# Optimization experiments

Hardware: AMD Instinct MI355X
Metric: run time of the kernel (lower is better)

## Reference

```python
import jax, jax.numpy as jnp
import numpy as np

B, S, D_IN, D_OUT, H = 4, 2048, 1024, 1024, 16
HD = D_OUT // H  # head_dim = 64


def setup_inputs() -> dict:
    key = jax.random.key(0)
    ks = jax.random.split(key, 9)
    sc_in = 1.0 / np.sqrt(D_IN)
    sc_out = 1.0 / np.sqrt(D_OUT)
    return {
        "x": jax.random.normal(ks[0], (B, S, D_IN), dtype=jnp.float32),
        "Wq": jax.random.normal(ks[1], (D_IN, D_OUT), dtype=jnp.float32) * sc_in,
        "bq": jax.random.normal(ks[2], (D_OUT,), dtype=jnp.float32) * 0.01,
        "Wk": jax.random.normal(ks[3], (D_IN, D_OUT), dtype=jnp.float32) * sc_in,
        "bk": jax.random.normal(ks[4], (D_OUT,), dtype=jnp.float32) * 0.01,
        "Wv": jax.random.normal(ks[5], (D_IN, D_OUT), dtype=jnp.float32) * sc_in,
        "bv": jax.random.normal(ks[6], (D_OUT,), dtype=jnp.float32) * 0.01,
        "Wo": jax.random.normal(ks[7], (D_OUT, D_OUT), dtype=jnp.float32) * sc_out,
        "bo": jax.random.normal(ks[8], (D_OUT,), dtype=jnp.float32) * 0.01,
    }


def reference(x, Wq, bq, Wk, bk, Wv, bv, Wo, bo):
    b, s, _ = x.shape
    # QKV projections -> [b, h, s, hd]
    def proj(W, bias):
        return (x @ W + bias).reshape(b, s, H, HD).transpose(0, 2, 1, 3)
    q, k, v = proj(Wq, bq), proj(Wk, bk), proj(Wv, bv)
    # scaled scores [b, h, s, s] with causal mask (future positions -> -inf)
    scores = jnp.einsum("bhqd,bhkd->bhqk", q, k) / jnp.sqrt(jnp.float32(HD))
    causal = jnp.triu(jnp.ones((s, s), dtype=bool), k=1)
    scores = jnp.where(causal, -jnp.inf, scores)
    attn = jax.nn.softmax(scores, axis=-1)  # dropout p=0.0 -> identity
    ctx = jnp.einsum("bhqk,bhkd->bhqd", attn, v)
    ctx = ctx.transpose(0, 2, 1, 3).reshape(b, s, D_OUT)
    return ctx @ Wo + bo
```

## Files before the change

### kernel.cpp

```cpp
#include <hip/hip_runtime.h>
#include <hip/hip_bf16.h>

#define B_   4
#define S_   2048
#define H_   16
#define HD_  64
#define D_   1024
#define M_   (B_ * S_)
#define N3_  3072

typedef unsigned short u16;
typedef __bf16 bf16x8 __attribute__((ext_vector_type(8)));
typedef float  f32x4  __attribute__((ext_vector_type(4)));
typedef unsigned short u16x8 __attribute__((ext_vector_type(8)));
typedef unsigned short u16x4 __attribute__((ext_vector_type(4)));

__device__ __forceinline__ float b2f(u16 u) {
    unsigned int x = ((unsigned int)u) << 16;
    return __builtin_bit_cast(float, x);
}
__device__ __forceinline__ u16 f2b(float f) {
    unsigned int x = __builtin_bit_cast(unsigned int, f);
    x += 0x7fffu + ((x >> 16) & 1u);
    return (u16)(x >> 16);
}
__device__ __forceinline__ u16 f2bt(float f) {
    return (u16)(__builtin_bit_cast(unsigned int, f) >> 16);
}

typedef const __attribute__((address_space(1))) unsigned int* gas_u32p;
typedef __attribute__((address_space(3))) unsigned int* las_u32p;
__device__ __forceinline__ void gl_lds16(const u16* g, u16* lds_base) {
    __builtin_amdgcn_global_load_lds((gas_u32p)g, (las_u32p)lds_base, 16, 0, 0);
}

__global__ __launch_bounds__(256) void cvt_k(const float* __restrict__ in,
                                             u16* __restrict__ out) {
    size_t i = ((size_t)blockIdx.x * 256 + threadIdx.x) * 8;
    float4 a = *(const float4*)(in + i);
    float4 b = *(const float4*)(in + i + 4);
    *(u16x8*)(out + i) = u16x8{f2b(a.x), f2b(a.y), f2b(a.z), f2b(a.w),
                               f2b(b.x), f2b(b.y), f2b(b.z), f2b(b.w)};
}

__global__ __launch_bounds__(256) void transpose4_k(
    const float* __restrict__ w0, const float* __restrict__ w1,
    const float* __restrict__ w2, const float* __restrict__ w3,
    u16* __restrict__ oqkv, u16* __restrict__ owo, float scale0) {
    __shared__ u16 t[32][33];
    const int z = blockIdx.z;
    const float* in = (z == 0) ? w0 : (z == 1) ? w1 : (z == 2) ? w2 : w3;
    u16* out = (z < 3) ? oqkv + (size_t)z * D_ * D_ : owo;
    const float sc = (z == 0) ? scale0 : 1.0f;
    const int x0 = blockIdx.x * 32, y0 = blockIdx.y * 32;
    const int tx = threadIdx.x & 31, ty = threadIdx.x >> 5;
#pragma unroll
    for (int i = 0; i < 32; i += 8)
        t[ty + i][tx] = f2b(in[(size_t)(y0 + ty + i) * D_ + x0 + tx] * sc);
    __syncthreads();
#pragma unroll
    for (int i = 0; i < 32; i += 8)
        out[(size_t)(x0 + ty + i) * D_ + y0 + tx] = t[tx][ty + i];
}

#define BM 128
#define BN 128
#define BK 64

template <int MODE>
__global__ __launch_bounds__(256) void gemm_core(
    const u16* __restrict__ A, const u16* __restrict__ Bt,
    const float* __restrict__ b0, const float* __restrict__ b1,
    const float* __restrict__ b2, float cscale,
    void* __restrict__ O0, void* __restrict__ O1, void* __restrict__ O2,
    int M, int N, int K)
{
    __shared__ __align__(16) u16 As[BM * BK];
    __shared__ __align__(16) u16 Bs[BN * BK];

    const int tid  = threadIdx.x;
    const int lane = tid & 63;
    const int wave = tid >> 6;
    const int wr = wave >> 1, wc = wave & 1;
    const int l15 = lane & 15, quad = lane >> 4;
    const int m0 = blockIdx.x * BM, n0 = blockIdx.y * BN;
    const int r8 = lane >> 3;
    const int csw = ((lane & 7) ^ r8) * 8;

    f32x4 acc[4][4] = {};

    for (int k0 = 0; k0 < K; k0 += BK) {
#pragma unroll
        for (int i = 0; i < 4; ++i) {
            const int row = wave * 32 + i * 8 + r8;
            gl_lds16(A  + (size_t)(m0 + row) * K + k0 + csw,
                     As + (wave * 32 + i * 8) * BK);
            gl_lds16(Bt + (size_t)(n0 + row) * K + k0 + csw,
                     Bs + (wave * 32 + i * 8) * BK);
        }
        __syncthreads();
        bf16x8 af[4][2], bfr[4][2];
#pragma unroll
        for (int t = 0; t < 4; ++t) {
            const u16* ap = As + (wr * 64 + t * 16 + l15) * BK;
            const u16* bp = Bs + (wc * 64 + t * 16 + l15) * BK;
            const int s7 = l15 & 7;
            af[t][0]  = *(const bf16x8*)(ap + ((quad    ) ^ s7) * 8);
            af[t][1]  = *(const bf16x8*)(ap + ((quad + 4) ^ s7) * 8);
            bfr[t][0] = *(const bf16x8*)(bp + ((quad    ) ^ s7) * 8);
            bfr[t][1] = *(const bf16x8*)(bp + ((quad + 4) ^ s7) * 8);
        }
#pragma unroll
        for (int mt = 0; mt < 4; ++mt)
#pragma unroll
            for (int nt = 0; nt < 4; ++nt) {
                acc[mt][nt] = __builtin_amdgcn_mfma_f32_16x16x32_bf16(
                    af[mt][0], bfr[nt][0], acc[mt][nt], 0, 0, 0);
                acc[mt][nt] = __builtin_amdgcn_mfma_f32_16x16x32_bf16(
                    af[mt][1], bfr[nt][1], acc[mt][nt], 0, 0, 0);
            }
        __syncthreads();
    }

#pragma unroll
    for (int nt = 0; nt < 4; ++nt) {
        const int col = n0 + wc * 64 + nt * 16 + l15;
        if constexpr (MODE == 1) {
            const float bv = b0[col];
#pragma unroll
            for (int mt = 0; mt < 4; ++mt) {
                const int rbase = m0 + wr * 64 + mt * 16 + quad * 4;
#pragma unroll
                for (int r2 = 0; r2 < 4; ++r2)
                    ((float*)O0)[(size_t)(rbase + r2) * N + col] =
                        acc[mt][nt][r2] + bv;
            }
        } else {
            const int qidx = col >> 10, ncol = col & (D_ - 1);
            const float bv = (qidx == 0) ? b0[ncol] * cscale
                           : (qidx == 1) ? b1[ncol] : b2[ncol];
#pragma unroll
            for (int mt = 0; mt < 4; ++mt) {
                const int rbase = m0 + wr * 64 + mt * 16 + quad * 4;
                if (qidx == 2) {
                    const int bidx = rbase >> 11, s = rbase & (S_ - 1);
                    const int hh = ncol >> 6, hd = ncol & 63;
                    u16x4 pk{f2b(acc[mt][nt][0] + bv), f2b(acc[mt][nt][1] + bv),
                             f2b(acc[mt][nt][2] + bv), f2b(acc[mt][nt][3] + bv)};
                    *(u16x4*)((u16*)O2 +
                        (((size_t)(bidx * H_ + hh)) * HD_ + hd) * S_ + s) = pk;
                } else {
                    u16* dst = (qidx == 0) ? (u16*)O0 : (u16*)O1;
#pragma unroll
                    for (int r2 = 0; r2 < 4; ++r2)
                        dst[(size_t)(rbase + r2) * D_ + ncol] =
                            f2b(acc[mt][nt][r2] + bv);
                }
            }
        }
    }
}

__global__ __launch_bounds__(256) void attn_mfma_k(
    const u16* __restrict__ Qm, const u16* __restrict__ Km,
    const u16* __restrict__ Vtg, u16* __restrict__ Om)
{
    __shared__ __align__(16) u16 Kbuf[2][64 * 64];
    __shared__ __align__(16) u16 Vbuf[2][64 * 64];
    __shared__ __align__(16) u16 Ps[4][16 * 64];

    const int tid  = threadIdx.x;
    const int lane = tid & 63;
    const int wave = tid >> 6;
    const int l15  = lane & 15;
    const int quad = lane >> 4;
    const int bh = blockIdx.x, b = bh >> 4, h = bh & (H_ - 1);
    const int j  = blockIdx.y;
    const int dg[4] = { j, 15 - j, 16 + j, 31 - j };

    const u16* Qg = Qm + (size_t)b * S_ * D_ + h * HD_;
    const u16* Kg = Km + (size_t)b * S_ * D_ + h * HD_;
    const u16* Vg = Vtg + ((size_t)(b * H_ + h)) * HD_ * S_;

    bf16x8 qf[4][2];
#pragma unroll
    for (int qs = 0; qs < 4; ++qs) {
        const u16* qp = Qg + (size_t)(dg[qs] * 64 + wave * 16 + l15) * D_ + quad * 8;
        qf[qs][0] = *(const bf16x8*)qp;
        qf[qs][1] = *(const bf16x8*)(qp + 32);
    }

    f32x4 of[4][4] = {};
    float lacc[4] = {0.f, 0.f, 0.f, 0.f};
    u16* pw = Ps[wave];
    const int qloc = wave * 16 + l15;
    const int r8 = lane >> 3;
    const int csw = ((lane & 7) ^ r8) * 8;

    auto stage = [&](int t, int bsel) {
        u16* kb = Kbuf[bsel];
        u16* vb = Vbuf[bsel];
#pragma unroll
        for (int i = 0; i < 2; ++i) {
            const int row = wave * 16 + i * 8 + r8;
            gl_lds16(Kg + (size_t)(t * 64 + row) * D_ + csw,
                     kb + (wave * 16 + i * 8) * 64);
            gl_lds16(Vg + (size_t)row * S_ + t * 64 + csw,
                     vb + (wave * 16 + i * 8) * 64);
        }
    };

    bf16x8 kf[4][2], vf[4][2];

    auto pass = [&](const bf16x8 (&q)[2], f32x4 (&o)[4], float& la, bool domask) {
        f32x4 sf[4];
#pragma unroll
        for (int kt = 0; kt < 4; ++kt) {
            f32x4 a = {};
            a = __builtin_amdgcn_mfma_f32_16x16x32_bf16(kf[kt][0], q[0], a, 0, 0, 0);
            a = __builtin_amdgcn_mfma_f32_16x16x32_bf16(kf[kt][1], q[1], a, 0, 0, 0);
            sf[kt] = a;
        }
        float ls = 0.f;
        u16 pb[16];
        if (domask) {
#pragma unroll
            for (int kt = 0; kt < 4; ++kt)
#pragma unroll
                for (int r = 0; r < 4; ++r) {
                    float v = sf[kt][r];
                    if (kt * 16 + quad * 4 + r > qloc) v = -INFINITY;
                    float p = __builtin_amdgcn_exp2f(v);
                    ls += p; pb[kt * 4 + r] = f2bt(p);
                }
        } else {
#pragma unroll
            for (int kt = 0; kt < 4; ++kt)
#pragma unroll
                for (int r = 0; r < 4; ++r) {
                    float p = __builtin_amdgcn_exp2f(sf[kt][r]);
                    ls += p; pb[kt * 4 + r] = f2bt(p);
                }
        }
        la += ls;
#pragma unroll
        for (int kt = 0; kt < 4; ++kt) {
            const int g = kt * 16 + quad * 4;
            const int pos = ((g >> 3) ^ (l15 & 7)) * 8 + (g & 7);
            *(u16x4*)(pw + l15 * 64 + pos) =
                u16x4{pb[kt * 4], pb[kt * 4 + 1], pb[kt * 4 + 2], pb[kt * 4 + 3]};
        }
        bf16x8 pf0 = *(const bf16x8*)(pw + l15 * 64 + ((quad    ) ^ (l15 & 7)) * 8);
        bf16x8 pf1 = *(const bf16x8*)(pw + l15 * 64 + ((quad + 4) ^ (l15 & 7)) * 8);
#pragma unroll
        for (int dt = 0; dt < 4; ++dt) {
            o[dt] = __builtin_amdgcn_mfma_f32_16x16x32_bf16(vf[dt][0], pf0, o[dt], 0, 0, 0);
            o[dt] = __builtin_amdgcn_mfma_f32_16x16x32_bf16(vf[dt][1], pf1, o[dt], 0, 0, 0);
        }
    };

    const int T = 32 - j;
    stage(0, 0);
    for (int t = 0; t < T; ++t) {
        __syncthreads();
        if (t + 1 < T) stage(t + 1, (t + 1) & 1);
        const u16* kb = Kbuf[t & 1];
        const u16* vb = Vbuf[t & 1];
#pragma unroll
        for (int kt = 0; kt < 4; ++kt) {
            const u16* kp = kb + (kt * 16 + l15) * 64;
            const u16* vp = vb + (kt * 16 + l15) * 64;
            const int s7 = l15 & 7;
            kf[kt][0] = *(const bf16x8*)(kp + ((quad    ) ^ s7) * 8);
            kf[kt][1] = *(const bf16x8*)(kp + ((quad + 4) ^ s7) * 8);
            vf[kt][0] = *(const bf16x8*)(vp + ((quad    ) ^ s7) * 8);
            vf[kt][1] = *(const bf16x8*)(vp + ((quad + 4) ^ s7) * 8);
        }
        if (t <= dg[0]) pass(qf[0], of[0], lacc[0], t == dg[0]);
        if (t <= dg[1]) pass(qf[1], of[1], lacc[1], t == dg[1]);
        if (t <= dg[2]) pass(qf[2], of[2], lacc[2], t == dg[2]);
        if (t <= dg[3]) pass(qf[3], of[3], lacc[3], t == dg[3]);
    }

    auto epi = [&](const f32x4 (&o)[4], float la, int dgq) {
        float ls = la;
        ls += __shfl_xor(ls, 16);
        ls += __shfl_xor(ls, 32);
        const float inv = 1.f / ls;
#pragma unroll
        for (int dt = 0; dt < 4; ++dt) {
            const int g = dt * 16 + quad * 4;
            const int pos = ((g >> 3) ^ (l15 & 7)) * 8 + (g & 7);
            *(u16x4*)(pw + l15 * 64 + pos) =
                u16x4{f2b(o[dt][0] * inv), f2b(o[dt][1] * inv),
                      f2b(o[dt][2] * inv), f2b(o[dt][3] * inv)};
        }
        const int r  = lane >> 2;
        const int cp = lane & 3;
        u16x8 o0 = *(const u16x8*)(pw + r * 64 + ((2 * cp    ) ^ (r & 7)) * 8);
        u16x8 o1 = *(const u16x8*)(pw + r * 64 + ((2 * cp + 1) ^ (r & 7)) * 8);
        u16* op = Om + ((size_t)(b * S_ + dgq * 64 + wave * 16 + r)) * D_ + h * 64 + cp * 16;
        *(u16x8*)op = o0;
        *(u16x8*)(op + 8) = o1;
    };
    epi(of[0], lacc[0], dg[0]);
    epi(of[1], lacc[1], dg[1]);
    epi(of[2], lacc[2], dg[2]);
    epi(of[3], lacc[3], dg[3]);
}

extern "C" void kernel_launch(void* const* d_in, const int* in_sizes, int n_in,
                              void* d_out, int out_size, void* d_ws, size_t ws_size,
                              hipStream_t stream)
{
    (void)in_sizes; (void)n_in; (void)out_size; (void)ws_size;
    const float* x  = (const float*)d_in[0];
    const float* Wq = (const float*)d_in[1];
    const float* bq = (const float*)d_in[2];
    const float* Wk = (const float*)d_in[3];
    const float* bk = (const float*)d_in[4];
    const float* Wv = (const float*)d_in[5];
    const float* bv = (const float*)d_in[6];
    const float* Wo = (const float*)d_in[7];
    const float* bo = (const float*)d_in[8];

    const float cscale = 0.18033688011112042f;

    u16* ws = (u16*)d_ws;
    const size_t MD = (size_t)M_ * D_;
    const size_t DD = (size_t)D_ * D_;
    u16* xb    = ws;
    u16* Qb    = xb + MD;
    u16* Kb    = Qb + MD;
    u16* Vtb   = Kb + MD;
    u16* Cb    = Vtb + MD;
    u16* WqkvT = Cb + MD;
    u16* WoT   = WqkvT + 3 * DD;

    cvt_k<<<M_ * D_ / 2048, 256, 0, stream>>>(x, xb);

    transpose4_k<<<dim3(D_ / 32, D_ / 32, 4), 256, 0, stream>>>(
        Wq, Wk, Wv, Wo, WqkvT, WoT, cscale);

    gemm_core<0><<<dim3(M_ / BM, N3_ / BN), 256, 0, stream>>>(
        xb, WqkvT, bq, bk, bv, cscale, Qb, Kb, Vtb, M_, N3_, D_);

    attn_mfma_k<<<dim3(B_ * H_, 8), 256, 0, stream>>>(Qb, Kb, Vtb, Cb);

    gemm_core<1><<<dim3(M_ / BM, D_ / BN), 256, 0, stream>>>(
        Cb, WoT, bo, nullptr, nullptr, 1.0f, d_out, nullptr, nullptr, M_, D_, D_);
}
```

Baseline: 291.0 us.

## Split attention into two query tiles per block and shuffle P in registers

Each attention block now handles two paired query tiles (j and 31-j) instead of four, and the grid doubles to 16 blocks along y, giving more blocks for the device to schedule. The probability matrix is packed two bf16 values per word and rearranged with cross-lane shuffles instead of a round trip through LDS. K/V fragments are loaded from LDS inside each pass rather than held in registers, and launch bounds request 4 blocks per CU to lower register pressure. The cost is more K/V LDS reads, since each tile is reloaded per pass, and each block streams the K/V tiles for fewer queries, so there is less reuse.

```diff
diff --git a/kernel.cpp b/kernel.cpp
--- a/kernel.cpp
+++ b/kernel.cpp
@@ -12,6 +12,7 @@
 typedef unsigned short u16;
 typedef __bf16 bf16x8 __attribute__((ext_vector_type(8)));
 typedef float  f32x4  __attribute__((ext_vector_type(4)));
+typedef int    i32x4  __attribute__((ext_vector_type(4)));
 typedef unsigned short u16x8 __attribute__((ext_vector_type(8)));
 typedef unsigned short u16x4 __attribute__((ext_vector_type(4)));
 
@@ -23,9 +24,6 @@
     unsigned int x = __builtin_bit_cast(unsigned int, f);
     x += 0x7fffu + ((x >> 16) & 1u);
     return (u16)(x >> 16);
-}
-__device__ __forceinline__ u16 f2bt(float f) {
-    return (u16)(__builtin_bit_cast(unsigned int, f) >> 16);
 }
 
 typedef const __attribute__((address_space(1))) unsigned int* gas_u32p;
@@ -161,7 +159,7 @@
     }
 }
 
-__global__ __launch_bounds__(256) void attn_mfma_k(
+__global__ __launch_bounds__(256, 4) void attn_mfma_k(
     const u16* __restrict__ Qm, const u16* __restrict__ Km,
     const u16* __restrict__ Vtg, u16* __restrict__ Om)
 {
@@ -174,28 +172,30 @@
     const int wave = tid >> 6;
     const int l15  = lane & 15;
     const int quad = lane >> 4;
+    const int s7   = l15 & 7;
     const int bh = blockIdx.x, b = bh >> 4, h = bh & (H_ - 1);
     const int j  = blockIdx.y;
-    const int dg[4] = { j, 15 - j, 16 + j, 31 - j };
+    const int dg0 = j, dg1 = 31 - j;
 
     const u16* Qg = Qm + (size_t)b * S_ * D_ + h * HD_;
     const u16* Kg = Km + (size_t)b * S_ * D_ + h * HD_;
     const u16* Vg = Vtg + ((size_t)(b * H_ + h)) * HD_ * S_;
 
-    bf16x8 qf[4][2];
-#pragma unroll
-    for (int qs = 0; qs < 4; ++qs) {
-        const u16* qp = Qg + (size_t)(dg[qs] * 64 + wave * 16 + l15) * D_ + quad * 8;
-        qf[qs][0] = *(const bf16x8*)qp;
-        qf[qs][1] = *(const bf16x8*)(qp + 32);
+    bf16x8 qf0[2], qf1[2];
+    {
+        const u16* qp = Qg + (size_t)(dg0 * 64 + wave * 16 + l15) * D_ + quad * 8;
+        qf0[0] = *(const bf16x8*)qp; qf0[1] = *(const bf16x8*)(qp + 32);
+        qp = Qg + (size_t)(dg1 * 64 + wave * 16 + l15) * D_ + quad * 8;
+        qf1[0] = *(const bf16x8*)qp; qf1[1] = *(const bf16x8*)(qp + 32);
     }
 
-    f32x4 of[4][4] = {};
-    float lacc[4] = {0.f, 0.f, 0.f, 0.f};
-    u16* pw = Ps[wave];
+    f32x4 of0[4] = {}, of1[4] = {};
+    float lacc0 = 0.f, lacc1 = 0.f;
     const int qloc = wave * 16 + l15;
     const int r8 = lane >> 3;
     const int csw = ((lane & 7) ^ r8) * 8;
+    const int srcA = l15 + ((quad & 1) << 5);
+    const int srcB = srcA + 16;
 
     auto stage = [&](int t, int bsel) {
         u16* kb = Kbuf[bsel];
@@ -210,52 +210,78 @@
         }
     };
 
-    bf16x8 kf[4][2], vf[4][2];
-
-    auto pass = [&](const bf16x8 (&q)[2], f32x4 (&o)[4], float& la, bool domask) {
+    auto pass = [&](const bf16x8 (&q)[2], f32x4 (&o)[4], float& la,
+                    bool domask, const u16* kb, const u16* vb) {
         f32x4 sf[4];
 #pragma unroll
         for (int kt = 0; kt < 4; ++kt) {
+            const u16* kp = kb + (kt * 16 + l15) * 64;
+            bf16x8 k0 = *(const bf16x8*)(kp + ((quad    ) ^ s7) * 8);
+            bf16x8 k1 = *(const bf16x8*)(kp + ((quad + 4) ^ s7) * 8);
             f32x4 a = {};
-            a = __builtin_amdgcn_mfma_f32_16x16x32_bf16(kf[kt][0], q[0], a, 0, 0, 0);
-            a = __builtin_amdgcn_mfma_f32_16x16x32_bf16(kf[kt][1], q[1], a, 0, 0, 0);
+            a = __builtin_amdgcn_mfma_f32_16x16x32_bf16(k0, q[0], a, 0, 0, 0);
+            a = __builtin_amdgcn_mfma_f32_16x16x32_bf16(k1, q[1], a, 0, 0, 0);
             sf[kt] = a;
         }
+        unsigned int w[4][2];
         float ls = 0.f;
-        u16 pb[16];
         if (domask) {
 #pragma unroll
             for (int kt = 0; kt < 4; ++kt)
 #pragma unroll
-                for (int r = 0; r < 4; ++r) {
-                    float v = sf[kt][r];
-                    if (kt * 16 + quad * 4 + r > qloc) v = -INFINITY;
-                    float p = __builtin_amdgcn_exp2f(v);
-                    ls += p; pb[kt * 4 + r] = f2bt(p);
+                for (int hh = 0; hh < 2; ++hh) {
+                    float v0 = sf[kt][2 * hh], v1 = sf[kt][2 * hh + 1];
+                    if (kt * 16 + quad * 4 + 2 * hh     > qloc) v0 = -INFINITY;
+                    if (kt * 16 + quad * 4 + 2 * hh + 1 > qloc) v1 = -INFINITY;
+                    float p0 = __builtin_amdgcn_exp2f(v0);
+                    float p1 = __builtin_amdgcn_exp2f(v1);
+                    ls += p0 + p1;
+                    w[kt][hh] = (__builtin_bit_cast(unsigned int, p0) >> 16) |
+                                (__builtin_bit_cast(unsigned int, p1) & 0xFFFF0000u);
                 }
         } else {
 #pragma unroll
             for (int kt = 0; kt < 4; ++kt)
 #pragma unroll
-                for (int r = 0; r < 4; ++r) {
-                    float p = __builtin_amdgcn_exp2f(sf[kt][r]);
-                    ls += p; pb[kt * 4 + r] = f2bt(p);
+                for (int hh = 0; hh < 2; ++hh) {
+                    float p0 = __builtin_amdgcn_exp2f(sf[kt][2 * hh]);
+                    float p1 = __builtin_amdgcn_exp2f(sf[kt][2 * hh + 1]);
+                    ls += p0 + p1;
+                    w[kt][hh] = (__builtin_bit_cast(unsigned int, p0) >> 16) |
+                                (__builtin_bit_cast(unsigned int, p1) & 0xFFFF0000u);
                 }
         }
         la += ls;
-#pragma unroll
-        for (int kt = 0; kt < 4; ++kt) {
-            const int g = kt * 16 + quad * 4;
-            const int pos = ((g >> 3) ^ (l15 & 7)) * 8 + (g & 7);
-            *(u16x4*)(pw + l15 * 64 + pos) =
-                u16x4{pb[kt * 4], pb[kt * 4 + 1], pb[kt * 4 + 2], pb[kt * 4 + 3]};
-        }
-        bf16x8 pf0 = *(const bf16x8*)(pw + l15 * 64 + ((quad    ) ^ (l15 & 7)) * 8);
-        bf16x8 pf1 = *(const bf16x8*)(pw + l15 * 64 + ((quad + 4) ^ (l15 & 7)) * 8);
+        const bool hi = (quad & 2) != 0;
+        i32x4 f0, f1;
+        {
+            int a0, a1;
+            a0 = __shfl((int)w[0][0], srcA); a1 = __shfl((int)w[1][0], srcA);
+            f0.x = hi ? a1 : a0;
+            a0 = __shfl((int)w[0][1], srcA); a1 = __shfl((int)w[1][1], srcA);
+            f0.y = hi ? a1 : a0;
+            a0 = __shfl((int)w[0][0], srcB); a1 = __shfl((int)w[1][0], srcB);
+            f0.z = hi ? a1 : a0;
+            a0 = __shfl((int)w[0][1], srcB); a1 = __shfl((int)w[1][1], srcB);
+            f0.w = hi ? a1 : a0;
+            a0 = __shfl((int)w[2][0], srcA); a1 = __shfl((int)w[3][0], srcA);
+            f1.x = hi ? a1 : a0;
+            a0 = __shfl((int)w[2][1], srcA); a1 = __shfl((int)w[3][1], srcA);
+            f1.y = hi ? a1 : a0;
+            a0 = __shfl((int)w[2][0], srcB); a1 = __shfl((int)w[3][0], srcB);
+            f1.z = hi ? a1 : a0;
+            a0 = __shfl((int)w[2][1], srcB); a1 = __shfl((int)w[3][1], srcB);
+            f1.w = hi ? a1 : a0;
+        }
+        bf16x8 pf0 = __builtin_bit_cast(bf16x8, f0);
+        bf16x8 pf1 = __builtin_bit_cast(bf16x8, f1);
 #pragma unroll
         for (int dt = 0; dt < 4; ++dt) {
-            o[dt] = __builtin_amdgcn_mfma_f32_16x16x32_bf16(vf[dt][0], pf0, o[dt], 0, 0, 0);
-            o[dt] = __builtin_amdgcn_mfma_f32_16x16x32_bf16(vf[dt][1], pf1, o[dt], 0, 0, 0);
+            const u16* vp = vb + (dt * 16 + l15) * 64;
+            bf16x8 v0 = *(const bf16x8*)(vp + ((quad    ) ^ s7) * 8);
+            bf16x8 v1 = *(const bf16x8*)(vp + ((quad + 4) ^ s7) * 8);
+            o[dt] = __builtin_amdgcn_mfma_f32_16x16x32_bf16(v0, pf0, o[dt], 0, 0, 0);
+            o[dt] = __builtin_amdgcn_mfma_f32_16x16x32_bf16(v1, pf1, o[dt], 0, 0, 0);
         }
     };
 
@@ -266,22 +292,11 @@
         if (t + 1 < T) stage(t + 1, (t + 1) & 1);
         const u16* kb = Kbuf[t & 1];
         const u16* vb = Vbuf[t & 1];
-#pragma unroll
-        for (int kt = 0; kt < 4; ++kt) {
-            const u16* kp = kb + (kt * 16 + l15) * 64;
-            const u16* vp = vb + (kt * 16 + l15) * 64;
-            const int s7 = l15 & 7;
-            kf[kt][0] = *(const bf16x8*)(kp + ((quad    ) ^ s7) * 8);
-            kf[kt][1] = *(const bf16x8*)(kp + ((quad + 4) ^ s7) * 8);
-            vf[kt][0] = *(const bf16x8*)(vp + ((quad    ) ^ s7) * 8);
-            vf[kt][1] = *(const bf16x8*)(vp + ((quad + 4) ^ s7) * 8);
-        }
-        if (t <= dg[0]) pass(qf[0], of[0], lacc[0], t == dg[0]);
-        if (t <= dg[1]) pass(qf[1], of[1], lacc[1], t == dg[1]);
-        if (t <= dg[2]) pass(qf[2], of[2], lacc[2], t == dg[2]);
-        if (t <= dg[3]) pass(qf[3], of[3], lacc[3], t == dg[3]);
+        if (t <= dg0) pass(qf0, of0, lacc0, t == dg0, kb, vb);
+        pass(qf1, of1, lacc1, t == dg1, kb, vb);
     }
 
+    u16* pw = Ps[wave];
     auto epi = [&](const f32x4 (&o)[4], float la, int dgq) {
         float ls = la;
         ls += __shfl_xor(ls, 16);
@@ -290,7 +305,7 @@
 #pragma unroll
         for (int dt = 0; dt < 4; ++dt) {
             const int g = dt * 16 + quad * 4;
-            const int pos = ((g >> 3) ^ (l15 & 7)) * 8 + (g & 7);
+            const int pos = ((g >> 3) ^ s7) * 8 + (g & 7);
             *(u16x4*)(pw + l15 * 64 + pos) =
                 u16x4{f2b(o[dt][0] * inv), f2b(o[dt][1] * inv),
                       f2b(o[dt][2] * inv), f2b(o[dt][3] * inv)};
@@ -303,10 +318,8 @@
         *(u16x8*)op = o0;
         *(u16x8*)(op + 8) = o1;
     };
-    epi(of[0], lacc[0], dg[0]);
-    epi(of[1], lacc[1], dg[1]);
-    epi(of[2], lacc[2], dg[2]);
-    epi(of[3], lacc[3], dg[3]);
+    epi(of0, lacc0, dg0);
+    epi(of1, lacc1, dg1);
 }
 
 extern "C" void kernel_launch(void* const* d_in, const int* in_sizes, int n_in,
@@ -345,7 +358,7 @@
     gemm_core<0><<<dim3(M_ / BM, N3_ / BN), 256, 0, stream>>>(
         xb, WqkvT, bq, bk, bv, cscale, Qb, Kb, Vtb, M_, N3_, D_);
 
-    attn_mfma_k<<<dim3(B_ * H_, 8), 256, 0, stream>>>(Qb, Kb, Vtb, Cb);
+    attn_mfma_k<<<dim3(B_ * H_, 16), 256, 0, stream>>>(Qb, Kb, Vtb, Cb);
 
     gemm_core<1><<<dim3(M_ / BM, D_ / BN), 256, 0, stream>>>(
         Cb, WoT, bo, nullptr, nullptr, 1.0f, d_out, nullptr, nullptr, M_, D_, D_);
```

Result: faster. 267.0 us (-8.2%).
